# Kernel tuning notes

Hardware: AMD Instinct MI355X
Metric: run time of the kernel (lower is better)

The kernel has to match this reference:

```python
import jax, jax.numpy as jnp
import numpy as np
import math

# Model/config constants (from LunarisCodexConfig defaults)
B, S, D = 4, 4096, 768
E = 8            # n_experts
TOP_K = 2
H = 2048         # SwiGLU hidden: multiple_of*ceil((2/3*4*768)/256)
CAP_F = 1.25     # capacity_factor
EPS = 1e-6       # RMSNorm eps
ALPHA = 1.0      # 1/sqrt(n_reasoning_steps), n_reasoning_steps=1


def setup_inputs() -> dict:
    key = jax.random.key(0)
    k0, k1, k2, k3 = jax.random.split(key, 4)
    x = jax.random.normal(k0, (B, S, D), jnp.float32)
    gate_w = jax.random.normal(k1, (E, D), jnp.float32) * 0.02          # router
    w13 = jax.random.normal(k2, (E, 2 * H, D), jnp.float32) * 0.02      # fused gate/up per expert
    w2 = jax.random.normal(k3, (E, D, H), jnp.float32) * 0.02           # down proj per expert
    norm_w = jnp.ones((E, D), jnp.float32)                              # per-expert RMSNorm weight
    return {"x": x, "gate_w": gate_w, "w13": w13, "w2": w2, "norm_w": norm_w}


def reference(x, gate_w, w13, w2, norm_w):
    Bx, Sx, Dx = x.shape
    N = Bx * Sx
    cap = int(math.ceil(CAP_F * TOP_K * N / E))
    xf = x.reshape(N, Dx)

    # ---- router in fp32, top-k gating with renormalized weights ----
    logits = xf.astype(jnp.float32) @ gate_w.T                 # [N, E]
    probs = jax.nn.softmax(logits, axis=-1)
    top_p, top_i = jax.lax.top_k(probs, TOP_K)                 # [N, K]
    w = top_p / jnp.sum(top_p, axis=-1, keepdims=True)         # [N, K]

    # ---- vectorized capacity-based dispatch (token-major, k-minor order) ----
    flat_e = top_i.reshape(-1)                                  # [N*K]
    onehot = jax.nn.one_hot(flat_e, E, dtype=jnp.int32)         # [N*K, E]
    pos = jnp.take_along_axis(jnp.cumsum(onehot, axis=0) - 1,
                              flat_e[:, None], axis=1)[:, 0]    # rank within expert
    keep = pos < cap                                            # capacity mask
    didx = flat_e * cap + jnp.minimum(pos, cap - 1)             # slot id in [0, E*cap)
    safe = jnp.where(keep, didx, E * cap)                       # dropped -> scratch row

    x_rep = jnp.repeat(xf, TOP_K, axis=0)                       # [N*K, D]
    buf = jnp.zeros((E * cap + 1, Dx), x.dtype).at[safe].set(x_rep)
    buf = buf[:-1].reshape(E, cap, Dx)                          # [E, C, D]

    z = 2.0 * buf
    z = z * jax.lax.rsqrt(jnp.mean(z * z, axis=-1, keepdims=True) + EPS)
    z = z * norm_w[:, None, :]
    gu = jnp.einsum('ecd,ehd->ech', z, w13)                     # [E, C, 2H]
    g, u = jnp.split(gu, 2, axis=-1)
    y = buf + ALPHA * jnp.einsum('ech,edh->ecd', jax.nn.silu(g) * u, w2)

    # ---- combine: gather back, weight, drop over-capacity slots ----
    y_tok = y.reshape(E * cap, Dx)[didx]                        # [N*K, D]
    cw = (w.reshape(-1) * keep.astype(w.dtype)).astype(x.dtype)
    out = (cw[:, None] * y_tok).reshape(N, TOP_K, Dx).sum(axis=1)
    return out.reshape(Bx, Sx, Dx)
```

## Files before the change

### kernel.cpp

```cpp
#include <hip/hip_runtime.h>
#include <hip/hip_bf16.h>
#include <stdint.h>


#define N_TOK 16384
#define D_    768
#define E_    8
#define H_    2048
#define CAP   5120
#define NK    (N_TOK * 2)
#define EPS_  1e-6f

typedef unsigned short u16;
typedef unsigned char  u8;
typedef __attribute__((ext_vector_type(8))) __bf16 v8bf;
typedef __attribute__((ext_vector_type(4))) float  v4f;

typedef __attribute__((address_space(3))) unsigned int lds_u32;
typedef const __attribute__((address_space(1))) unsigned int glb_u32;

__device__ __forceinline__ void gload16(const void* g, void* lds) {
    __builtin_amdgcn_global_load_lds((glb_u32*)g, (lds_u32*)lds, 16, 0, 0);
}

__device__ __forceinline__ float bf2f(u16 u) {
    union { uint32_t i; float f; } v; v.i = ((uint32_t)u) << 16; return v.f;
}
__device__ __forceinline__ u16 f2bf(float f) {
    union { uint32_t i; float f; } v; v.f = f;
    uint32_t r = v.i + 0x7fffu + ((v.i >> 16) & 1u);
    return (u16)(r >> 16);
}

__global__ __launch_bounds__(256) void conv_bf16_kernel(
    const float* __restrict__ src, u16* __restrict__ dst, int n4)
{
    for (int i = blockIdx.x * 256 + threadIdx.x; i < n4; i += gridDim.x * 256) {
        float4 v = ((const float4*)src)[i];
        ushort4 o;
        o.x = f2bf(v.x); o.y = f2bf(v.y); o.z = f2bf(v.z); o.w = f2bf(v.w);
        ((ushort4*)dst)[i] = o;
    }
}

__global__ __launch_bounds__(256) void router_kernel(
    const float* __restrict__ x, const float* __restrict__ gate_w,
    int* __restrict__ routerEx, float* __restrict__ routerW)
{
    __shared__ float gw[E_ * D_];
    int t = threadIdx.x;
    for (int i = t; i < E_ * D_; i += 256) gw[i] = gate_w[i];
    __syncthreads();
    int wv = t >> 6, l = t & 63;
    int n = blockIdx.x * 4 + wv;
    const float* xr = x + (size_t)n * D_;
    float p[E_];
#pragma unroll
    for (int e = 0; e < E_; ++e) p[e] = 0.f;
#pragma unroll
    for (int j = 0; j < 12; ++j) {
        int d = l + 64 * j;
        float xv = xr[d];
#pragma unroll
        for (int e = 0; e < E_; ++e) p[e] += xv * gw[e * D_ + d];
    }
#pragma unroll
    for (int off = 32; off > 0; off >>= 1) {
#pragma unroll
        for (int e = 0; e < E_; ++e) p[e] += __shfl_xor(p[e], off, 64);
    }
    if (l == 0) {
        int e0 = 0; float m0 = p[0];
#pragma unroll
        for (int e = 1; e < E_; ++e) if (p[e] > m0) { m0 = p[e]; e0 = e; }
        int e1 = (e0 == 0) ? 1 : 0; float m1 = p[e1];
#pragma unroll
        for (int e = 0; e < E_; ++e) if (e != e0 && p[e] > m1) { m1 = p[e]; e1 = e; }
        float w0 = 1.f / (1.f + __expf(m1 - m0));
        routerEx[2 * n] = e0; routerEx[2 * n + 1] = e1;
        routerW[2 * n] = w0; routerW[2 * n + 1] = 1.f - w0;
    }
}

__global__ __launch_bounds__(256) void dispatch_kernel(
    const int* __restrict__ routerEx, int* __restrict__ tokenSlot,
    int* __restrict__ slotToken, int* __restrict__ cnt)
{
    __shared__ u8  exs[NK + NK / 128];
    __shared__ int hist[256 * E_];
    int t = threadIdx.x;
    for (int i = t; i < NK; i += 256)
        exs[i + (i >> 7)] = (u8)routerEx[i];
    __syncthreads();
    int loc[E_];
#pragma unroll
    for (int e = 0; e < E_; ++e) loc[e] = 0;
    int abase = t * 129;
    for (int j = 0; j < NK / 256; ++j) {
        int ev = exs[abase + j];
#pragma unroll
        for (int e = 0; e < E_; ++e) loc[e] += (ev == e) ? 1 : 0;
    }
#pragma unroll
    for (int e = 0; e < E_; ++e) hist[t * E_ + e] = loc[e];
    __syncthreads();
    if (t < E_) {
        int run = 0;
        for (int tt = 0; tt < 256; ++tt) { int v = hist[tt * E_ + t]; hist[tt * E_ + t] = run; run += v; }
        cnt[t] = run;
    }
    __syncthreads();
    int off[E_];
#pragma unroll
    for (int e = 0; e < E_; ++e) off[e] = hist[t * E_ + e];
    int base = t * (NK / 256);
    for (int j = 0; j < NK / 256; ++j) {
        int i = base + j;
        int ev = exs[abase + j];
        int pos = 0;
#pragma unroll
        for (int e = 0; e < E_; ++e) { if (ev == e) { pos = off[e]; off[e] = pos + 1; } }
        if (pos < CAP) {
            int s = ev * CAP + pos;
            tokenSlot[i] = s;
            slotToken[s] = i;
        } else {
            tokenSlot[i] = -1;
        }
    }
}

__global__ __launch_bounds__(256) void init_out_kernel(
    const float* __restrict__ x, const int* __restrict__ tokenSlot,
    const float* __restrict__ routerW, float* __restrict__ out)
{
    int g = blockIdx.x * 256 + threadIdx.x;
    int n = g / 96;
    int d0 = (g - n * 96) * 8;
    float w0 = (tokenSlot[2 * n] >= 0) ? routerW[2 * n] : 0.f;
    float w1 = (tokenSlot[2 * n + 1] >= 0) ? routerW[2 * n + 1] : 0.f;
    float ws = w0 + w1;
    const float* xr = x + (size_t)n * D_ + d0;
    float* orow = out + (size_t)n * D_ + d0;
    float4 a = *(const float4*)&xr[0];
    float4 b = *(const float4*)&xr[4];
    float4 oa, ob;
    oa.x = ws * a.x; oa.y = ws * a.y; oa.z = ws * a.z; oa.w = ws * a.w;
    ob.x = ws * b.x; ob.y = ws * b.y; ob.z = ws * b.z; ob.w = ws * b.w;
    *(float4*)&orow[0] = oa;
    *(float4*)&orow[4] = ob;
}

__global__ __launch_bounds__(256) void gather_norm_kernel(
    const float* __restrict__ x, const float* __restrict__ norm_w,
    const int* __restrict__ slotToken, const int* __restrict__ cnt,
    u16* __restrict__ zAll, size_t zStride, int eFixed)
{
    int e = eFixed + blockIdx.z;
    u16* zE = zAll + (size_t)blockIdx.z * zStride;
    int t = threadIdx.x, wv = t >> 6, l = t & 63;
    int pos = blockIdx.x * 4 + wv;
    int ce = min(cnt[e], CAP);
    u16* zr = zE + (size_t)pos * D_;
    if (pos >= ce) {
        ushort4 zz = { 0, 0, 0, 0 };
#pragma unroll
        for (int j = 0; j < 3; ++j) *(ushort4*)&zr[l * 4 + 256 * j] = zz;
        return;
    }
    int tok = slotToken[e * CAP + pos] >> 1;
    const float* xr = x + (size_t)tok * D_;
    float xv[12]; float ss = 0.f;
#pragma unroll
    for (int j = 0; j < 3; ++j) {
        float4 v4 = *(const float4*)&xr[l * 4 + 256 * j];
        xv[4 * j] = v4.x; xv[4 * j + 1] = v4.y; xv[4 * j + 2] = v4.z; xv[4 * j + 3] = v4.w;
        ss += v4.x * v4.x + v4.y * v4.y + v4.z * v4.z + v4.w * v4.w;
    }
#pragma unroll
    for (int off = 32; off > 0; off >>= 1) ss += __shfl_xor(ss, off, 64);
    float rs = rsqrtf(4.f * ss * (1.f / (float)D_) + EPS_);
    const float* nw = norm_w + e * D_;
#pragma unroll
    for (int j = 0; j < 3; ++j) {
        int d0 = l * 4 + 256 * j;
        float4 nv = *(const float4*)&nw[d0];
        ushort4 o;
        o.x = f2bf(2.f * xv[4 * j]     * rs * nv.x);
        o.y = f2bf(2.f * xv[4 * j + 1] * rs * nv.y);
        o.z = f2bf(2.f * xv[4 * j + 2] * rs * nv.z);
        o.w = f2bf(2.f * xv[4 * j + 3] * rs * nv.w);
        *(ushort4*)&zr[d0] = o;
    }
}

#define STAGE(tk) do { int b3_ = (tk) & 3; size_t ko_ = (size_t)(tk) * 64; \
    u16* A_ = &lds[b3_][0][0]; u16* B_ = &lds[b3_][1][0]; \
    gload16(aS0 + ko_, A_ + w * 512); \
    gload16(aS1 + ko_, A_ + 4096 + w * 512); \
    gload16(bS0 + ko_, B_ + w * 512); \
    gload16(bS1 + ko_, B_ + 4096 + w * 512); } while (0)

#define PIPE_WAIT_BARRIER(tk, NT) do { \
    if ((tk) + 3 < (NT))      asm volatile("s_waitcnt vmcnt(8)" ::: "memory"); \
    else if ((tk) + 2 < (NT)) asm volatile("s_waitcnt vmcnt(4)" ::: "memory"); \
    else if ((tk) + 1 < (NT)) asm volatile("s_waitcnt vmcnt(0)" ::: "memory"); \
    if ((tk) + 1 < (NT)) { __builtin_amdgcn_s_barrier(); __builtin_amdgcn_sched_barrier(0); } } while (0)

__global__ __launch_bounds__(512, 2) void gemm1_kernel(
    const u16* __restrict__ zAll, size_t zStride,
    const u16* __restrict__ w13All, size_t wStride,
    u16* __restrict__ actAll, size_t actStride,
    const int* __restrict__ cnt, int eFixed)
{
    int hw  = blockIdx.y * 16 + blockIdx.x;
    int xcd = hw & 7, cid = hw >> 3;
    int jn  = (xcd & 3) * 4 + (cid & 3);
    int rb  = (xcd >> 2) * 10 + (cid >> 2);
    int e   = eFixed + blockIdx.z;
    int ce  = min(cnt[e], CAP);
    if (rb * 256 >= ce) return;
    const u16* zE   = zAll   + (size_t)blockIdx.z * zStride;
    const u16* w13e = w13All + (size_t)blockIdx.z * wStride;
    u16*       actE = actAll + (size_t)blockIdx.z * actStride;

    __shared__ __align__(16) u16 lds[4][2][8192];

    int t = threadIdx.x, w = t >> 6, l = t & 63;
    int wr = w >> 2, wc = w & 3;

    int srow = t >> 2;
    int ssw  = (((t & 3) ^ ((t >> 3) & 3)) << 4);
    const char* aS0 = (const char*)(zE + (size_t)(rb * 256 + srow) * D_) + ssw;
    const char* aS1 = aS0 + (size_t)128 * D_ * 2;
    const char* bS0 = (const char*)(w13e + (size_t)(jn * 128 + srow) * D_) + ssw;
    const char* bS1 = (const char*)(w13e + (size_t)(H_ + jn * 128 + srow) * D_) + ssw;

    int fr = l & 15, slot = l >> 4;
    int swz  = (slot ^ ((fr >> 1) & 3)) << 4;
    int aoff = (wr * 128 + fr) * 64 + swz;
    int boff = (wc * 32 + fr) * 64 + swz;

    const v4f vzero = { 0.f, 0.f, 0.f, 0.f };
    v4f acc[8][4];
#pragma unroll
    for (int i = 0; i < 8; ++i)
#pragma unroll
        for (int j = 0; j < 4; ++j) acc[i][j] = vzero;

    STAGE(0); STAGE(1); STAGE(2);
    asm volatile("s_waitcnt vmcnt(8)" ::: "memory");
    __builtin_amdgcn_s_barrier();
    __builtin_amdgcn_sched_barrier(0);

#pragma unroll 1
    for (int tk = 0; tk < 24; ++tk) {
        if (tk + 3 < 24) STAGE(tk + 3);
        __builtin_amdgcn_sched_barrier(0);
        const char* A3 = (const char*)&lds[tk & 3][0][0];
        const char* B3 = (const char*)&lds[tk & 3][1][0];
        v8bf bv[4], a0_[4], a1_[4];
#pragma unroll
        for (int cg = 0; cg < 4; ++cg)
            bv[cg] = *(const v8bf*)(B3 + boff + ((cg & 1) * 1024 + (cg >> 1) * 8192));
#pragma unroll
        for (int rg = 0; rg < 4; ++rg) a0_[rg] = *(const v8bf*)(A3 + aoff + rg * 1024);
        __builtin_amdgcn_s_setprio(1);
#pragma unroll
        for (int rg = 0; rg < 4; ++rg)
#pragma unroll
            for (int cg = 0; cg < 4; ++cg)
                acc[rg][cg] = __builtin_amdgcn_mfma_f32_16x16x32_bf16(a0_[rg], bv[cg], acc[rg][cg], 0, 0, 0);
        __builtin_amdgcn_s_setprio(0);
#pragma unroll
        for (int rg = 0; rg < 4; ++rg) a1_[rg] = *(const v8bf*)(A3 + aoff + (rg + 4) * 1024);
        __builtin_amdgcn_s_setprio(1);
#pragma unroll
        for (int rg = 0; rg < 4; ++rg)
#pragma unroll
            for (int cg = 0; cg < 4; ++cg)
                acc[rg + 4][cg] = __builtin_amdgcn_mfma_f32_16x16x32_bf16(a1_[rg], bv[cg], acc[rg + 4][cg], 0, 0, 0);
        __builtin_amdgcn_s_setprio(0);
        PIPE_WAIT_BARRIER(tk, 24);
    }

    __syncthreads();
    u16* ep = (u16*)&lds[0][0][0];
    int rquad = (l >> 4) * 4;
#pragma unroll
    for (int rg = 0; rg < 8; ++rg) {
#pragma unroll
        for (int cg = 0; cg < 2; ++cg) {
            v4f g = acc[rg][cg], u = acc[rg][cg + 2];
#pragma unroll
            for (int r = 0; r < 4; ++r) {
                int row = wr * 128 + rg * 16 + rquad + r;
                int col = wc * 32 + cg * 16 + fr;
                float gv = g[r];
                ep[row * 136 + col] = f2bf(gv / (1.f + __expf(-gv)) * u[r]);
            }
        }
    }
    __syncthreads();
#pragma unroll
    for (int i = 0; i < 8; ++i) {
        int idx = i * 512 + t;
        int row = idx >> 4, c8 = (idx & 15) << 3;
        uint4 v = *(const uint4*)&ep[row * 136 + c8];
        *(uint4*)&actE[(size_t)(rb * 256 + row) * H_ + jn * 128 + c8] = v;
    }
}

template <bool WRITE_DELTA>
__global__ __launch_bounds__(512, 2) void gemm2_kernel(
    const u16* __restrict__ actAll, size_t actStride,
    const u16* __restrict__ w2All, size_t wStride,
    const int* __restrict__ slotToken, const float* __restrict__ routerW,
    float* __restrict__ out, u16* __restrict__ deltaAll, size_t deltaStride,
    const int* __restrict__ cnt, int eFixed)
{
    int jn = blockIdx.x;
    int rb = blockIdx.y;
    int e  = eFixed + blockIdx.z;
    int ce = min(cnt[e], CAP);
    if (rb * 256 >= ce) return;
    const u16* actE = actAll + (size_t)blockIdx.z * actStride;
    const u16* w2e  = w2All  + (size_t)blockIdx.z * wStride;

    __shared__ __align__(16) u16 lds[4][2][8192];

    int t = threadIdx.x, w = t >> 6, l = t & 63;
    int wr = w >> 2, wc = w & 3;

    int srow = t >> 2;
    int ssw  = (((t & 3) ^ ((t >> 3) & 3)) << 4);
    const char* aS0 = (const char*)(actE + (size_t)(rb * 256 + srow) * H_) + ssw;
    const char* aS1 = aS0 + (size_t)128 * H_ * 2;
    const char* bS0 = (const char*)(w2e + (size_t)(jn * 256 + srow) * H_) + ssw;
    const char* bS1 = bS0 + (size_t)128 * H_ * 2;

    int fr = l & 15, slot = l >> 4;
    int swz  = (slot ^ ((fr >> 1) & 3)) << 4;
    int aoff = (wr * 128 + fr) * 64 + swz;
    int boff = (wc * 64 + fr) * 64 + swz;

    const v4f vzero = { 0.f, 0.f, 0.f, 0.f };
    v4f acc[8][4];
#pragma unroll
    for (int i = 0; i < 8; ++i)
#pragma unroll
        for (int j = 0; j < 4; ++j) acc[i][j] = vzero;

    STAGE(0); STAGE(1); STAGE(2);
    asm volatile("s_waitcnt vmcnt(8)" ::: "memory");
    __builtin_amdgcn_s_barrier();
    __builtin_amdgcn_sched_barrier(0);

#pragma unroll 1
    for (int tk = 0; tk < 64; ++tk) {
        if (tk + 3 < 64) STAGE(tk + 3);
        __builtin_amdgcn_sched_barrier(0);
        const char* A3 = (const char*)&lds[tk & 3][0][0];
        const char* B3 = (const char*)&lds[tk & 3][1][0];
        v8bf bv[4], a0_[4], a1_[4];
#pragma unroll
        for (int cg = 0; cg < 4; ++cg)
            bv[cg] = *(const v8bf*)(B3 + boff + cg * 1024);
#pragma unroll
        for (int rg = 0; rg < 4; ++rg) a0_[rg] = *(const v8bf*)(A3 + aoff + rg * 1024);
        __builtin_amdgcn_s_setprio(1);
#pragma unroll
        for (int rg = 0; rg < 4; ++rg)
#pragma unroll
            for (int cg = 0; cg < 4; ++cg)
                acc[rg][cg] = __builtin_amdgcn_mfma_f32_16x16x32_bf16(a0_[rg], bv[cg], acc[rg][cg], 0, 0, 0);
        __builtin_amdgcn_s_setprio(0);
#pragma unroll
        for (int rg = 0; rg < 4; ++rg) a1_[rg] = *(const v8bf*)(A3 + aoff + (rg + 4) * 1024);
        __builtin_amdgcn_s_setprio(1);
#pragma unroll
        for (int rg = 0; rg < 4; ++rg)
#pragma unroll
            for (int cg = 0; cg < 4; ++cg)
                acc[rg + 4][cg] = __builtin_amdgcn_mfma_f32_16x16x32_bf16(a1_[rg], bv[cg], acc[rg + 4][cg], 0, 0, 0);
        __builtin_amdgcn_s_setprio(0);
        PIPE_WAIT_BARRIER(tk, 64);
    }

    __syncthreads();
    u16* ep = (u16*)&lds[0][0][0];
    int rquad = (l >> 4) * 4;
#pragma unroll
    for (int h = 0; h < 2; ++h) {
        if (h) __syncthreads();
        if (wr == h) {
#pragma unroll
            for (int rg = 0; rg < 8; ++rg) {
#pragma unroll
                for (int cg = 0; cg < 4; ++cg) {
                    v4f a = acc[rg][cg];
#pragma unroll
                    for (int r = 0; r < 4; ++r) {
                        int row = rg * 16 + rquad + r;
                        int col = wc * 64 + cg * 16 + fr;
                        ep[row * 264 + col] = f2bf(a[r]);
                    }
                }
            }
        }
        __syncthreads();
        if (WRITE_DELTA) {
            u16* deltaE = deltaAll + (size_t)blockIdx.z * deltaStride;
#pragma unroll
            for (int i = 0; i < 8; ++i) {
                int idx = i * 512 + t;
                int row = idx >> 5, c8 = (idx & 31) << 3;
                uint4 v = *(const uint4*)&ep[row * 264 + c8];
                *(uint4*)&deltaE[(size_t)(rb * 256 + h * 128 + row) * D_ + jn * 256 + c8] = v;
            }
        } else {
#pragma unroll
            for (int i = 0; i < 16; ++i) {
                int idx = i * 512 + t;
                int row = idx >> 6, c = (idx & 63) << 2;
                int grow = rb * 256 + h * 128 + row;
                if (grow >= ce) continue;
                int sidx = slotToken[e * CAP + grow];
                int tok = sidx >> 1;
                float wg = routerW[sidx];
                const u16* dr = &ep[row * 264 + c];
                float* orow = out + (size_t)tok * D_ + jn * 256 + c;
                float4 cur = *(const float4*)orow;
                cur.x += wg * bf2f(dr[0]);
                cur.y += wg * bf2f(dr[1]);
                cur.z += wg * bf2f(dr[2]);
                cur.w += wg * bf2f(dr[3]);
                *(float4*)orow = cur;
            }
        }
    }
}

__global__ __launch_bounds__(256) void combine_kernel(
    const float* __restrict__ x, const u16* __restrict__ deltaBuf,
    const int* __restrict__ tokenSlot, const float* __restrict__ routerW,
    float* __restrict__ out)
{
    int g = blockIdx.x * 256 + threadIdx.x;
    int n = g / 192;
    int d0 = (g - n * 192) * 4;
    int s0 = tokenSlot[2 * n], s1 = tokenSlot[2 * n + 1];
    float w0 = (s0 >= 0) ? routerW[2 * n] : 0.f;
    float w1 = (s1 >= 0) ? routerW[2 * n + 1] : 0.f;
    float ws = w0 + w1;
    float4 xv = *(const float4*)&x[(size_t)n * D_ + d0];
    float4 o;
    o.x = ws * xv.x; o.y = ws * xv.y; o.z = ws * xv.z; o.w = ws * xv.w;
    if (s0 >= 0) {
        ushort4 dv = *(const ushort4*)&deltaBuf[(size_t)s0 * D_ + d0];
        o.x += w0 * bf2f(dv.x); o.y += w0 * bf2f(dv.y);
        o.z += w0 * bf2f(dv.z); o.w += w0 * bf2f(dv.w);
    }
    if (s1 >= 0) {
        ushort4 dv = *(const ushort4*)&deltaBuf[(size_t)s1 * D_ + d0];
        o.x += w1 * bf2f(dv.x); o.y += w1 * bf2f(dv.y);
        o.z += w1 * bf2f(dv.z); o.w += w1 * bf2f(dv.w);
    }
    *(float4*)&out[(size_t)n * D_ + d0] = o;
}

extern "C" void kernel_launch(void* const* d_in, const int* in_sizes, int n_in,
                              void* d_out, int out_size, void* d_ws, size_t ws_size,
                              hipStream_t stream)
{
    (void)in_sizes; (void)n_in; (void)out_size;
    const float* x      = (const float*)d_in[0];
    const float* gate_w = (const float*)d_in[1];
    const float* w13    = (const float*)d_in[2];
    const float* w2     = (const float*)d_in[3];
    const float* norm_w = (const float*)d_in[4];
    float* out = (float*)d_out;

    const size_t zSlice   = (size_t)CAP * D_ * 2;
    const size_t actSlice = (size_t)CAP * H_ * 2;
    const size_t w13Slice = (size_t)2 * H_ * D_ * 2;
    const size_t w2Slice  = (size_t)D_ * H_ * 2;
    const size_t ctrl     = (size_t)NK * 4 * 3 + (size_t)E_ * CAP * 4 + 256;

    char* ws = (char*)d_ws;
    size_t off = 0;
    int*   routerEx  = (int*)(ws + off);   off += (size_t)NK * 4;
    float* routerW   = (float*)(ws + off); off += (size_t)NK * 4;
    int*   tokenSlot = (int*)(ws + off);   off += (size_t)NK * 4;
    int*   slotToken = (int*)(ws + off);   off += (size_t)E_ * CAP * 4;
    int*   cnt       = (int*)(ws + off);   off += 256;

    const size_t bigNeed = ctrl + E_ * (zSlice + actSlice + w13Slice + w2Slice) + E_ * zSlice ;
    bool batched = ws_size >= bigNeed;

    router_kernel<<<N_TOK / 4, 256, 0, stream>>>(x, gate_w, routerEx, routerW);
    dispatch_kernel<<<1, 256, 0, stream>>>(routerEx, tokenSlot, slotToken, cnt);

    if (batched) {
        u16* zBuf     = (u16*)(ws + off); off += E_ * zSlice;
        u16* actBuf   = (u16*)(ws + off); off += E_ * actSlice;
        u16* deltaBuf = (u16*)(ws + off); off += E_ * zSlice;
        u16* w13bf    = (u16*)(ws + off); off += E_ * w13Slice;
        u16* w2bf     = (u16*)(ws + off); off += E_ * w2Slice;

        int n13 = E_ * 2 * H_ * D_ / 4, n2 = E_ * D_ * H_ / 4;
        conv_bf16_kernel<<<(n13 + 255) / 256, 256, 0, stream>>>(w13, w13bf, n13);
        conv_bf16_kernel<<<(n2 + 255) / 256, 256, 0, stream>>>(w2, w2bf, n2);
        gather_norm_kernel<<<dim3(CAP / 4, 1, E_), 256, 0, stream>>>(
            x, norm_w, slotToken, cnt, zBuf, zSlice / 2, 0);
        gemm1_kernel<<<dim3(16, CAP / 256, E_), 512, 0, stream>>>(
            zBuf, zSlice / 2, w13bf, w13Slice / 2, actBuf, actSlice / 2, cnt, 0);
        gemm2_kernel<true><<<dim3(3, CAP / 256, E_), 512, 0, stream>>>(
            actBuf, actSlice / 2, w2bf, w2Slice / 2, slotToken, routerW,
            out, deltaBuf, zSlice / 2, cnt, 0);
        combine_kernel<<<(N_TOK * (D_ / 4)) / 256, 256, 0, stream>>>(
            x, deltaBuf, tokenSlot, routerW, out);
    } else {
        u16* zE   = (u16*)(ws + off); off += zSlice;
        u16* actE = (u16*)(ws + off); off += actSlice;
        u16* w13e = (u16*)(ws + off); off += w13Slice;
        u16* w2e  = (u16*)(ws + off); off += w2Slice;

        init_out_kernel<<<(N_TOK * (D_ / 8)) / 256, 256, 0, stream>>>(x, tokenSlot, routerW, out);
        int n13 = 2 * H_ * D_ / 4, n2 = D_ * H_ / 4;
        for (int e = 0; e < E_; ++e) {
            conv_bf16_kernel<<<(n13 + 255) / 256, 256, 0, stream>>>(
                w13 + (size_t)e * 2 * H_ * D_, w13e, n13);
            conv_bf16_kernel<<<(n2 + 255) / 256, 256, 0, stream>>>(
                w2 + (size_t)e * D_ * H_, w2e, n2);
            gather_norm_kernel<<<dim3(CAP / 4, 1, 1), 256, 0, stream>>>(
                x, norm_w, slotToken, cnt, zE, 0, e);
            gemm1_kernel<<<dim3(16, CAP / 256, 1), 512, 0, stream>>>(
                zE, 0, w13e, 0, actE, 0, cnt, e);
            gemm2_kernel<false><<<dim3(3, CAP / 256, 1), 512, 0, stream>>>(
                actE, 0, w2e, 0, slotToken, routerW, out, (u16*)nullptr, 0, cnt, e);
        }
    }
}
```

Measured before the change: 749.0 us.

## Split tile prefetch into A/B halves interleaved with barrier-synced MFMA phases

Splits the global-to-LDS staging of each K-tile into separate A and B halves and issues them between the LDS fragment reads and the two MFMA phases of each iteration. Extra workgroup barriers plus lgkmcnt waits are added so all waves move through phases in lockstep, in the style of a ping-pong schedule, aiming to spread memory issue and keep waves from contending. The cost is three extra barriers per K-step, which may stall waves and reduce the overlap between MFMA and loads.

```diff
diff --git a/kernel.cpp b/kernel.cpp
--- a/kernel.cpp
+++ b/kernel.cpp
@@ -194,12 +194,20 @@
     }
 }
 
-#define STAGE(tk) do { int b3_ = (tk) & 3; size_t ko_ = (size_t)(tk) * 64; \
-    u16* A_ = &lds[b3_][0][0]; u16* B_ = &lds[b3_][1][0]; \
+#define STAGE_A(tk) do { int b3_ = (tk) & 3; size_t ko_ = (size_t)(tk) * 64; \
+    u16* A_ = &lds[b3_][0][0]; \
     gload16(aS0 + ko_, A_ + w * 512); \
-    gload16(aS1 + ko_, A_ + 4096 + w * 512); \
+    gload16(aS1 + ko_, A_ + 4096 + w * 512); } while (0)
+
+#define STAGE_B(tk) do { int b3_ = (tk) & 3; size_t ko_ = (size_t)(tk) * 64; \
+    u16* B_ = &lds[b3_][1][0]; \
     gload16(bS0 + ko_, B_ + w * 512); \
     gload16(bS1 + ko_, B_ + 4096 + w * 512); } while (0)
+
+#define PHASE_SYNC() do { \
+    __builtin_amdgcn_s_barrier(); \
+    asm volatile("s_waitcnt lgkmcnt(0)" ::: "memory"); \
+    __builtin_amdgcn_sched_barrier(0); } while (0)
 
 #define PIPE_WAIT_BARRIER(tk, NT) do { \
     if ((tk) + 3 < (NT))      asm volatile("s_waitcnt vmcnt(8)" ::: "memory"); \
@@ -248,15 +256,13 @@
 #pragma unroll
         for (int j = 0; j < 4; ++j) acc[i][j] = vzero;
 
-    STAGE(0); STAGE(1); STAGE(2);
+    STAGE_A(0); STAGE_B(0); STAGE_A(1); STAGE_B(1); STAGE_A(2); STAGE_B(2);
     asm volatile("s_waitcnt vmcnt(8)" ::: "memory");
     __builtin_amdgcn_s_barrier();
     __builtin_amdgcn_sched_barrier(0);
 
 #pragma unroll 1
     for (int tk = 0; tk < 24; ++tk) {
-        if (tk + 3 < 24) STAGE(tk + 3);
-        __builtin_amdgcn_sched_barrier(0);
         const char* A3 = (const char*)&lds[tk & 3][0][0];
         const char* B3 = (const char*)&lds[tk & 3][1][0];
         v8bf bv[4], a0_[4], a1_[4];
@@ -265,6 +271,8 @@
             bv[cg] = *(const v8bf*)(B3 + boff + ((cg & 1) * 1024 + (cg >> 1) * 8192));
 #pragma unroll
         for (int rg = 0; rg < 4; ++rg) a0_[rg] = *(const v8bf*)(A3 + aoff + rg * 1024);
+        if (tk + 3 < 24) STAGE_A(tk + 3);
+        PHASE_SYNC();
         __builtin_amdgcn_s_setprio(1);
 #pragma unroll
         for (int rg = 0; rg < 4; ++rg)
@@ -272,8 +280,11 @@
             for (int cg = 0; cg < 4; ++cg)
                 acc[rg][cg] = __builtin_amdgcn_mfma_f32_16x16x32_bf16(a0_[rg], bv[cg], acc[rg][cg], 0, 0, 0);
         __builtin_amdgcn_s_setprio(0);
+        __builtin_amdgcn_s_barrier();
 #pragma unroll
         for (int rg = 0; rg < 4; ++rg) a1_[rg] = *(const v8bf*)(A3 + aoff + (rg + 4) * 1024);
+        if (tk + 3 < 24) STAGE_B(tk + 3);
+        PHASE_SYNC();
         __builtin_amdgcn_s_setprio(1);
 #pragma unroll
         for (int rg = 0; rg < 4; ++rg)
@@ -351,15 +362,13 @@
 #pragma unroll
         for (int j = 0; j < 4; ++j) acc[i][j] = vzero;
 
-    STAGE(0); STAGE(1); STAGE(2);
+    STAGE_A(0); STAGE_B(0); STAGE_A(1); STAGE_B(1); STAGE_A(2); STAGE_B(2);
     asm volatile("s_waitcnt vmcnt(8)" ::: "memory");
     __builtin_amdgcn_s_barrier();
     __builtin_amdgcn_sched_barrier(0);
 
 #pragma unroll 1
     for (int tk = 0; tk < 64; ++tk) {
-        if (tk + 3 < 64) STAGE(tk + 3);
-        __builtin_amdgcn_sched_barrier(0);
         const char* A3 = (const char*)&lds[tk & 3][0][0];
         const char* B3 = (const char*)&lds[tk & 3][1][0];
         v8bf bv[4], a0_[4], a1_[4];
@@ -368,6 +377,8 @@
             bv[cg] = *(const v8bf*)(B3 + boff + cg * 1024);
 #pragma unroll
         for (int rg = 0; rg < 4; ++rg) a0_[rg] = *(const v8bf*)(A3 + aoff + rg * 1024);
+        if (tk + 3 < 64) STAGE_A(tk + 3);
+        PHASE_SYNC();
         __builtin_amdgcn_s_setprio(1);
 #pragma unroll
         for (int rg = 0; rg < 4; ++rg)
@@ -375,8 +386,11 @@
             for (int cg = 0; cg < 4; ++cg)
                 acc[rg][cg] = __builtin_amdgcn_mfma_f32_16x16x32_bf16(a0_[rg], bv[cg], acc[rg][cg], 0, 0, 0);
         __builtin_amdgcn_s_setprio(0);
+        __builtin_amdgcn_s_barrier();
 #pragma unroll
         for (int rg = 0; rg < 4; ++rg) a1_[rg] = *(const v8bf*)(A3 + aoff + (rg + 4) * 1024);
+        if (tk + 3 < 64) STAGE_B(tk + 3);
+        PHASE_SYNC();
         __builtin_amdgcn_s_setprio(1);
 #pragma unroll
         for (int rg = 0; rg < 4; ++rg)
```

Measured after the change: 743.5 us. No clear change (-0.7%).

## Replace multi-stage pipelined GEMM loops with single-buffer K=64 tiles

Applied to the files above, without the earlier changes.

Both expert GEMM kernels drop the four-deep async LDS prefetch pipeline. They now use a single-buffered loop that loads a 256x64 A/B tile, synchronises, and computes. Shared memory per block halves, and the epilogues are chunked to fit the smaller buffer. The gemm1 block-to-tile mapping across XCDs is also changed. In exchange, global loads no longer overlap the MFMA work, which risks exposed memory latency and extra barriers.

```diff
diff --git a/kernel.cpp b/kernel.cpp
--- a/kernel.cpp
+++ b/kernel.cpp
@@ -194,19 +194,6 @@
     }
 }
 
-#define STAGE(tk) do { int b3_ = (tk) & 3; size_t ko_ = (size_t)(tk) * 64; \
-    u16* A_ = &lds[b3_][0][0]; u16* B_ = &lds[b3_][1][0]; \
-    gload16(aS0 + ko_, A_ + w * 512); \
-    gload16(aS1 + ko_, A_ + 4096 + w * 512); \
-    gload16(bS0 + ko_, B_ + w * 512); \
-    gload16(bS1 + ko_, B_ + 4096 + w * 512); } while (0)
-
-#define PIPE_WAIT_BARRIER(tk, NT) do { \
-    if ((tk) + 3 < (NT))      asm volatile("s_waitcnt vmcnt(8)" ::: "memory"); \
-    else if ((tk) + 2 < (NT)) asm volatile("s_waitcnt vmcnt(4)" ::: "memory"); \
-    else if ((tk) + 1 < (NT)) asm volatile("s_waitcnt vmcnt(0)" ::: "memory"); \
-    if ((tk) + 1 < (NT)) { __builtin_amdgcn_s_barrier(); __builtin_amdgcn_sched_barrier(0); } } while (0)
-
 __global__ __launch_bounds__(512, 2) void gemm1_kernel(
     const u16* __restrict__ zAll, size_t zStride,
     const u16* __restrict__ w13All, size_t wStride,
@@ -215,8 +202,8 @@
 {
     int hw  = blockIdx.y * 16 + blockIdx.x;
     int xcd = hw & 7, cid = hw >> 3;
-    int jn  = (xcd & 3) * 4 + (cid & 3);
-    int rb  = (xcd >> 2) * 10 + (cid >> 2);
+    int jn  = xcd * 2 + cid / 20;
+    int rb  = cid % 20;
     int e   = eFixed + blockIdx.z;
     int ce  = min(cnt[e], CAP);
     if (rb * 256 >= ce) return;
@@ -224,22 +211,22 @@
     const u16* w13e = w13All + (size_t)blockIdx.z * wStride;
     u16*       actE = actAll + (size_t)blockIdx.z * actStride;
 
-    __shared__ __align__(16) u16 lds[4][2][8192];
+    __shared__ __align__(16) u16 smem[2 * 256 * 64];
+    u16* As = smem;
+    u16* Bs = smem + 256 * 64;
 
     int t = threadIdx.x, w = t >> 6, l = t & 63;
     int wr = w >> 2, wc = w & 3;
-
-    int srow = t >> 2;
-    int ssw  = (((t & 3) ^ ((t >> 3) & 3)) << 4);
-    const char* aS0 = (const char*)(zE + (size_t)(rb * 256 + srow) * D_) + ssw;
-    const char* aS1 = aS0 + (size_t)128 * D_ * 2;
-    const char* bS0 = (const char*)(w13e + (size_t)(jn * 128 + srow) * D_) + ssw;
-    const char* bS1 = (const char*)(w13e + (size_t)(H_ + jn * 128 + srow) * D_) + ssw;
-
-    int fr = l & 15, slot = l >> 4;
-    int swz  = (slot ^ ((fr >> 1) & 3)) << 4;
-    int aoff = (wr * 128 + fr) * 64 + swz;
-    int boff = (wc * 32 + fr) * 64 + swz;
+    int lr  = l >> 3;
+    int lsw = ((l & 7) ^ lr) << 4;
+
+    const char* aSrc = (const char*)(zE + (size_t)(rb * 256 + w * 32 + lr) * D_) + lsw;
+    int grow0 = ((w < 4) ? (jn * 128 + w * 32) : (H_ + jn * 128 + (w - 4) * 32)) + lr;
+    const char* bSrc = (const char*)(w13e + (size_t)grow0 * D_) + lsw;
+
+    int fr = l & 15;
+    int sw = (l & 7) << 4;
+    int fq = (l >> 4) << 4;
 
     const v4f vzero = { 0.f, 0.f, 0.f, 0.f };
     v4f acc[8][4];
@@ -248,66 +235,64 @@
 #pragma unroll
         for (int j = 0; j < 4; ++j) acc[i][j] = vzero;
 
-    STAGE(0); STAGE(1); STAGE(2);
-    asm volatile("s_waitcnt vmcnt(8)" ::: "memory");
-    __builtin_amdgcn_s_barrier();
-    __builtin_amdgcn_sched_barrier(0);
-
-#pragma unroll 1
-    for (int tk = 0; tk < 24; ++tk) {
-        if (tk + 3 < 24) STAGE(tk + 3);
-        __builtin_amdgcn_sched_barrier(0);
-        const char* A3 = (const char*)&lds[tk & 3][0][0];
-        const char* B3 = (const char*)&lds[tk & 3][1][0];
-        v8bf bv[4], a0_[4], a1_[4];
-#pragma unroll
-        for (int cg = 0; cg < 4; ++cg)
-            bv[cg] = *(const v8bf*)(B3 + boff + ((cg & 1) * 1024 + (cg >> 1) * 8192));
-#pragma unroll
-        for (int rg = 0; rg < 4; ++rg) a0_[rg] = *(const v8bf*)(A3 + aoff + rg * 1024);
-        __builtin_amdgcn_s_setprio(1);
-#pragma unroll
-        for (int rg = 0; rg < 4; ++rg)
-#pragma unroll
-            for (int cg = 0; cg < 4; ++cg)
-                acc[rg][cg] = __builtin_amdgcn_mfma_f32_16x16x32_bf16(a0_[rg], bv[cg], acc[rg][cg], 0, 0, 0);
-        __builtin_amdgcn_s_setprio(0);
-#pragma unroll
-        for (int rg = 0; rg < 4; ++rg) a1_[rg] = *(const v8bf*)(A3 + aoff + (rg + 4) * 1024);
-        __builtin_amdgcn_s_setprio(1);
-#pragma unroll
-        for (int rg = 0; rg < 4; ++rg)
-#pragma unroll
-            for (int cg = 0; cg < 4; ++cg)
-                acc[rg + 4][cg] = __builtin_amdgcn_mfma_f32_16x16x32_bf16(a1_[rg], bv[cg], acc[rg + 4][cg], 0, 0, 0);
-        __builtin_amdgcn_s_setprio(0);
-        PIPE_WAIT_BARRIER(tk, 24);
-    }
-
+    for (int kb = 0; kb < 12; ++kb) {
+        __syncthreads();
+#pragma unroll
+        for (int i = 0; i < 4; ++i) {
+            gload16(aSrc + i * (8 * D_ * 2), &As[(w * 32 + i * 8) * 64]);
+            gload16(bSrc + i * (8 * D_ * 2), &Bs[(w * 32 + i * 8) * 64]);
+        }
+        aSrc += 128; bSrc += 128;
+        __syncthreads();
+#pragma unroll
+        for (int ks = 0; ks < 2; ++ks) {
+            int kby = (ks * 64 + fq) ^ sw;
+            v8bf bv[4], av[8];
+#pragma unroll
+            for (int cg = 0; cg < 4; ++cg) {
+                int brow = ((cg < 2) ? (wc * 32 + cg * 16) : (128 + wc * 32 + (cg - 2) * 16)) + fr;
+                bv[cg] = *(const v8bf*)((const char*)Bs + brow * 128 + kby);
+            }
+#pragma unroll
+            for (int rg = 0; rg < 8; ++rg)
+                av[rg] = *(const v8bf*)((const char*)As + (wr * 128 + rg * 16 + fr) * 128 + kby);
+#pragma unroll
+            for (int rg = 0; rg < 8; ++rg)
+#pragma unroll
+                for (int cg = 0; cg < 4; ++cg)
+                    acc[rg][cg] = __builtin_amdgcn_mfma_f32_16x16x32_bf16(av[rg], bv[cg], acc[rg][cg], 0, 0, 0);
+        }
+    }
     __syncthreads();
-    u16* ep = (u16*)&lds[0][0][0];
+    u16* ep = smem;
     int rquad = (l >> 4) * 4;
 #pragma unroll
-    for (int rg = 0; rg < 8; ++rg) {
-#pragma unroll
-        for (int cg = 0; cg < 2; ++cg) {
-            v4f g = acc[rg][cg], u = acc[rg][cg + 2];
-#pragma unroll
-            for (int r = 0; r < 4; ++r) {
-                int row = wr * 128 + rg * 16 + rquad + r;
-                int col = wc * 32 + cg * 16 + fr;
-                float gv = g[r];
-                ep[row * 136 + col] = f2bf(gv / (1.f + __expf(-gv)) * u[r]);
+    for (int h = 0; h < 2; ++h) {
+        if (h) __syncthreads();
+        if (wr == h) {
+#pragma unroll
+            for (int rg = 0; rg < 8; ++rg) {
+#pragma unroll
+                for (int cg = 0; cg < 2; ++cg) {
+                    v4f g = acc[rg][cg], u = acc[rg][cg + 2];
+#pragma unroll
+                    for (int r = 0; r < 4; ++r) {
+                        int row = rg * 16 + rquad + r;
+                        int col = wc * 32 + cg * 16 + fr;
+                        float gv = g[r];
+                        ep[row * 136 + col] = f2bf(gv / (1.f + __expf(-gv)) * u[r]);
+                    }
+                }
             }
         }
-    }
-    __syncthreads();
-#pragma unroll
-    for (int i = 0; i < 8; ++i) {
-        int idx = i * 512 + t;
-        int row = idx >> 4, c8 = (idx & 15) << 3;
-        uint4 v = *(const uint4*)&ep[row * 136 + c8];
-        *(uint4*)&actE[(size_t)(rb * 256 + row) * H_ + jn * 128 + c8] = v;
+        __syncthreads();
+#pragma unroll
+        for (int i = 0; i < 4; ++i) {
+            int idx = i * 512 + t;
+            int row = idx >> 4, c8 = (idx & 15) << 3;
+            uint4 v = *(const uint4*)&ep[row * 136 + c8];
+            *(uint4*)&actE[(size_t)(rb * 256 + h * 128 + row) * H_ + jn * 128 + c8] = v;
+        }
     }
 }
 
@@ -327,22 +312,21 @@
     const u16* actE = actAll + (size_t)blockIdx.z * actStride;
     const u16* w2e  = w2All  + (size_t)blockIdx.z * wStride;
 
-    __shared__ __align__(16) u16 lds[4][2][8192];
+    __shared__ __align__(16) u16 smem[2 * 256 * 64];
+    u16* As = smem;
+    u16* Bs = smem + 256 * 64;
 
     int t = threadIdx.x, w = t >> 6, l = t & 63;
     int wr = w >> 2, wc = w & 3;
-
-    int srow = t >> 2;
-    int ssw  = (((t & 3) ^ ((t >> 3) & 3)) << 4);
-    const char* aS0 = (const char*)(actE + (size_t)(rb * 256 + srow) * H_) + ssw;
-    const char* aS1 = aS0 + (size_t)128 * H_ * 2;
-    const char* bS0 = (const char*)(w2e + (size_t)(jn * 256 + srow) * H_) + ssw;
-    const char* bS1 = bS0 + (size_t)128 * H_ * 2;
-
-    int fr = l & 15, slot = l >> 4;
-    int swz  = (slot ^ ((fr >> 1) & 3)) << 4;
-    int aoff = (wr * 128 + fr) * 64 + swz;
-    int boff = (wc * 64 + fr) * 64 + swz;
+    int lr  = l >> 3;
+    int lsw = ((l & 7) ^ lr) << 4;
+
+    const char* aSrc = (const char*)(actE + (size_t)(rb * 256 + w * 32 + lr) * H_) + lsw;
+    const char* bSrc = (const char*)(w2e + (size_t)(jn * 256 + w * 32 + lr) * H_) + lsw;
+
+    int fr = l & 15;
+    int sw = (l & 7) << 4;
+    int fq = (l >> 4) << 4;
 
     const v4f vzero = { 0.f, 0.f, 0.f, 0.f };
     v4f acc[8][4];
@@ -351,57 +335,48 @@
 #pragma unroll
         for (int j = 0; j < 4; ++j) acc[i][j] = vzero;
 
-    STAGE(0); STAGE(1); STAGE(2);
-    asm volatile("s_waitcnt vmcnt(8)" ::: "memory");
-    __builtin_amdgcn_s_barrier();
-    __builtin_amdgcn_sched_barrier(0);
-
-#pragma unroll 1
-    for (int tk = 0; tk < 64; ++tk) {
-        if (tk + 3 < 64) STAGE(tk + 3);
-        __builtin_amdgcn_sched_barrier(0);
-        const char* A3 = (const char*)&lds[tk & 3][0][0];
-        const char* B3 = (const char*)&lds[tk & 3][1][0];
-        v8bf bv[4], a0_[4], a1_[4];
-#pragma unroll
-        for (int cg = 0; cg < 4; ++cg)
-            bv[cg] = *(const v8bf*)(B3 + boff + cg * 1024);
-#pragma unroll
-        for (int rg = 0; rg < 4; ++rg) a0_[rg] = *(const v8bf*)(A3 + aoff + rg * 1024);
-        __builtin_amdgcn_s_setprio(1);
-#pragma unroll
-        for (int rg = 0; rg < 4; ++rg)
+    for (int kb = 0; kb < 32; ++kb) {
+        __syncthreads();
+#pragma unroll
+        for (int i = 0; i < 4; ++i) {
+            gload16(aSrc + i * (8 * H_ * 2), &As[(w * 32 + i * 8) * 64]);
+            gload16(bSrc + i * (8 * H_ * 2), &Bs[(w * 32 + i * 8) * 64]);
+        }
+        aSrc += 128; bSrc += 128;
+        __syncthreads();
+#pragma unroll
+        for (int ks = 0; ks < 2; ++ks) {
+            int kby = (ks * 64 + fq) ^ sw;
+            v8bf bv[4], av[8];
 #pragma unroll
             for (int cg = 0; cg < 4; ++cg)
-                acc[rg][cg] = __builtin_amdgcn_mfma_f32_16x16x32_bf16(a0_[rg], bv[cg], acc[rg][cg], 0, 0, 0);
-        __builtin_amdgcn_s_setprio(0);
-#pragma unroll
-        for (int rg = 0; rg < 4; ++rg) a1_[rg] = *(const v8bf*)(A3 + aoff + (rg + 4) * 1024);
-        __builtin_amdgcn_s_setprio(1);
-#pragma unroll
-        for (int rg = 0; rg < 4; ++rg)
-#pragma unroll
-            for (int cg = 0; cg < 4; ++cg)
-                acc[rg + 4][cg] = __builtin_amdgcn_mfma_f32_16x16x32_bf16(a1_[rg], bv[cg], acc[rg + 4][cg], 0, 0, 0);
-        __builtin_amdgcn_s_setprio(0);
-        PIPE_WAIT_BARRIER(tk, 64);
-    }
-
+                bv[cg] = *(const v8bf*)((const char*)Bs + (wc * 64 + cg * 16 + fr) * 128 + kby);
+#pragma unroll
+            for (int rg = 0; rg < 8; ++rg)
+                av[rg] = *(const v8bf*)((const char*)As + (wr * 128 + rg * 16 + fr) * 128 + kby);
+#pragma unroll
+            for (int rg = 0; rg < 8; ++rg)
+#pragma unroll
+                for (int cg = 0; cg < 4; ++cg)
+                    acc[rg][cg] = __builtin_amdgcn_mfma_f32_16x16x32_bf16(av[rg], bv[cg], acc[rg][cg], 0, 0, 0);
+        }
+    }
     __syncthreads();
-    u16* ep = (u16*)&lds[0][0][0];
+    u16* ep = smem;
     int rquad = (l >> 4) * 4;
 #pragma unroll
-    for (int h = 0; h < 2; ++h) {
-        if (h) __syncthreads();
-        if (wr == h) {
-#pragma unroll
-            for (int rg = 0; rg < 8; ++rg) {
+    for (int q = 0; q < 4; ++q) {
+        if (q) __syncthreads();
+        if (wr == (q >> 1)) {
+#pragma unroll
+            for (int rgq = 0; rgq < 4; ++rgq) {
+                int rg = (q & 1) * 4 + rgq;
 #pragma unroll
                 for (int cg = 0; cg < 4; ++cg) {
                     v4f a = acc[rg][cg];
 #pragma unroll
                     for (int r = 0; r < 4; ++r) {
-                        int row = rg * 16 + rquad + r;
+                        int row = rgq * 16 + rquad + r;
                         int col = wc * 64 + cg * 16 + fr;
                         ep[row * 264 + col] = f2bf(a[r]);
                     }
@@ -412,18 +387,18 @@
         if (WRITE_DELTA) {
             u16* deltaE = deltaAll + (size_t)blockIdx.z * deltaStride;
 #pragma unroll
-            for (int i = 0; i < 8; ++i) {
+            for (int i = 0; i < 4; ++i) {
                 int idx = i * 512 + t;
                 int row = idx >> 5, c8 = (idx & 31) << 3;
                 uint4 v = *(const uint4*)&ep[row * 264 + c8];
-                *(uint4*)&deltaE[(size_t)(rb * 256 + h * 128 + row) * D_ + jn * 256 + c8] = v;
+                *(uint4*)&deltaE[(size_t)(rb * 256 + q * 64 + row) * D_ + jn * 256 + c8] = v;
             }
         } else {
 #pragma unroll
-            for (int i = 0; i < 16; ++i) {
+            for (int i = 0; i < 8; ++i) {
                 int idx = i * 512 + t;
                 int row = idx >> 6, c = (idx & 63) << 2;
-                int grow = rb * 256 + h * 128 + row;
+                int grow = rb * 256 + q * 64 + row;
                 if (grow >= ce) continue;
                 int sidx = slotToken[e * CAP + grow];
                 int tok = sidx >> 1;
```

After: 845.0 us. 1.13x slower.
